# Kernel tuning notes

Hardware: AMD Instinct MI355X
Metric: run time of the kernel (lower is better)

## Reference

```python
import jax, jax.numpy as jnp
import numpy as np

NUM_EXPERTS = 32
TOP_K = 8
HIDDEN = 1536
INTER = 512


def setup_inputs() -> dict:
    key = jax.random.key(0)
    k1, k2, k3, k4 = jax.random.split(key, 4)
    hidden_states = jax.random.normal(k1, (4, 2048, HIDDEN), dtype=jnp.float32)
    # gate (router) weight: [E, H] as in nn.Linear(hidden, num_experts)
    gate_w = jax.random.normal(k2, (NUM_EXPERTS, HIDDEN), dtype=jnp.float32) * 0.02
    # fused gate+up projection per expert: [E, 2*I, H] (first I rows = gate/silu path)
    w13 = jax.random.normal(k3, (NUM_EXPERTS, 2 * INTER, HIDDEN), dtype=jnp.float32) * 0.02
    # down projection per expert: [E, H, I]
    w2 = jax.random.normal(k4, (NUM_EXPERTS, HIDDEN, INTER), dtype=jnp.float32) * 0.02
    return {"hidden_states": hidden_states, "gate_w": gate_w, "w13": w13, "w2": w2}


def _moe_forward(x, gate_w, w13, w2):
    orig_shape = x.shape
    x = x.reshape(-1, HIDDEN)            # [T, H]
    T = x.shape[0]

    # Router: softmax over all experts, then top-k, then renormalize.
    router_logits = x @ gate_w.T          # [T, E]
    probs = jax.nn.softmax(router_logits, axis=-1)
    topk_w, topk_idx = jax.lax.top_k(probs, TOP_K)        # [T, K]
    topk_w = topk_w / jnp.sum(topk_w, axis=-1, keepdims=True)

    # Scatter top-k weights into a dense [T, E] combine matrix (zeros elsewhere).
    expert_w = jnp.zeros((T, NUM_EXPERTS), dtype=x.dtype)
    expert_w = expert_w.at[jnp.arange(T)[:, None], topk_idx].add(topk_w)
    expert_w_eT = expert_w.T              # [E, T]

    def body(acc, ew):
        we, w13_e, w2_e = ew              # [T], [2I, H], [H, I]
        gu = x @ w13_e.T                  # [T, 2I]
        g, u = gu[:, :INTER], gu[:, INTER:]
        y = (jax.nn.silu(g) * u) @ w2_e.T  # [T, H]
        return acc + we[:, None] * y, None

    out, _ = jax.lax.scan(body, jnp.zeros_like(x), (expert_w_eT, w13, w2))
    return out.reshape(orig_shape)


def reference(hidden_states, gate_w, w13, w2):
    return _moe_forward(hidden_states, gate_w, w13, w2)
```

## Files before the change

kernel.cpp:

```cpp
#include <hip/hip_runtime.h>
#include <hip/hip_bf16.h>
#include <math.h>

#define NUM_EXPERTS 32
#define TOP_K 8
#define HIDDEN 1536
#define INTER 512

typedef __bf16 bf16_t;
typedef __bf16 bf16x8 __attribute__((ext_vector_type(8)));
typedef __bf16 bf16x4 __attribute__((ext_vector_type(4)));
typedef float f32x4 __attribute__((ext_vector_type(4)));

#define M_COUNTS    0
#define M_OFFSETS   32
#define M_CURSORS   96
#define M_NUMTILES  128
#define M_TILE_E    256
#define M_TILE_M0   1024
#define M_TILE_ROWS 2048
#define META_BYTES  16384

__device__ __forceinline__ void gld16(void* lds, const void* gsrc) {
  __builtin_amdgcn_global_load_lds(
      (const __attribute__((address_space(1))) void*)gsrc,
      (__attribute__((address_space(3))) void*)lds, 16, 0, 0);
}

__global__ __launch_bounds__(256) void k_cvt(
    const float* __restrict__ src, bf16_t* __restrict__ dst)
{
  size_t i = ((size_t)blockIdx.x * 256 + threadIdx.x) * 4;
  f32x4 v = *(const f32x4*)(src + i);
  bf16x4 o;
  o[0] = (bf16_t)v[0]; o[1] = (bf16_t)v[1]; o[2] = (bf16_t)v[2]; o[3] = (bf16_t)v[3];
  *(bf16x4*)(dst + i) = o;
}

__global__ __launch_bounds__(256) void k_tgw(
    const float* __restrict__ gw, float* __restrict__ gwT4)
{
  int tid = blockIdx.x * 256 + threadIdx.x;
  int e = tid / HIDDEN, k = tid % HIDDEN;
  gwT4[(k >> 2) * 128 + (e << 2) + (k & 3)] = gw[tid];
}

__global__ __launch_bounds__(64) void k_router(
    const float* __restrict__ x, const float* __restrict__ gwT4,
    int* __restrict__ meta, int* __restrict__ topk_idx, float* __restrict__ topk_w,
    bf16_t* __restrict__ x16)
{
  int t = blockIdx.x;
  int lane = threadIdx.x;
  int e = lane & 31, part = lane >> 5;
  const float* xrow = x + (size_t)t * HIDDEN;
  const f32x4* xr = (const f32x4*)(xrow + part * 768);
  const f32x4* gr = (const f32x4*)(gwT4 + part * 192 * 128 + e * 4);
  float s = 0.f;
#pragma unroll 4
  for (int i = 0; i < 192; ++i) {
    f32x4 xv = xr[i];
    f32x4 gv = gr[i * 32];
    s += xv[0] * gv[0] + xv[1] * gv[1] + xv[2] * gv[2] + xv[3] * gv[3];
  }
  s += __shfl_xor(s, 32);

  {
    const f32x4* xv4 = (const f32x4*)(xrow + lane * 24);
    bf16_t* xo = x16 + (size_t)t * HIDDEN + lane * 24;
#pragma unroll
    for (int i = 0; i < 6; ++i) {
      f32x4 v = xv4[i];
      bf16x4 o;
      o[0] = (bf16_t)v[0]; o[1] = (bf16_t)v[1]; o[2] = (bf16_t)v[2]; o[3] = (bf16_t)v[3];
      *(bf16x4*)(xo + i * 4) = o;
    }
  }

  float logit = s, rem = s;
  float m0 = 0.f, wsum = 0.f, my_l = 0.f;
  int my_e = 0;
#pragma unroll
  for (int k = 0; k < TOP_K; ++k) {
    float mx = rem;
#pragma unroll
    for (int off = 32; off >= 1; off >>= 1) mx = fmaxf(mx, __shfl_xor(mx, off));
    unsigned long long bal = __ballot(rem == mx);
    int src = __ffsll(bal) - 1;
    int ex = src & 31;
    float lv = __shfl(logit, ex);
    if (k == 0) m0 = mx;
    wsum += __expf(lv - m0);
    if (lane == k) { my_e = ex; my_l = lv; }
    if ((lane & 31) == ex) rem = -1e30f;
  }
  if (lane < TOP_K) {
    topk_idx[t * TOP_K + lane] = my_e;
    topk_w[t * TOP_K + lane] = __expf(my_l - m0) / wsum;
    atomicAdd(&meta[M_COUNTS + my_e], 1);
  }
}

__global__ void k_scan(int* __restrict__ meta)
{
  if (threadIdx.x != 0 || blockIdx.x != 0) return;
  int off = 0, nt = 0;
  for (int e = 0; e < NUM_EXPERTS; ++e) {
    int n = meta[M_COUNTS + e];
    meta[M_OFFSETS + e] = off;
    meta[M_CURSORS + e] = off;
    int tn = (n + 127) >> 7;
    for (int i = 0; i < tn; ++i) {
      meta[M_TILE_E + nt] = e;
      meta[M_TILE_M0 + nt] = off + i * 128;
      meta[M_TILE_ROWS + nt] = min(128, n - i * 128);
      ++nt;
    }
    off += n;
  }
  meta[M_OFFSETS + NUM_EXPERTS] = off;
  meta[M_NUMTILES] = nt;
}

__global__ __launch_bounds__(256) void k_scatter(
    const int* __restrict__ topk_idx,
    int* __restrict__ meta, int* __restrict__ pair_token, int* __restrict__ pair_pos)
{
  int i = blockIdx.x * 256 + threadIdx.x;
  int e = topk_idx[i];
  int pos = atomicAdd(&meta[M_CURSORS + e], 1);
  pair_token[pos] = i >> 3;
  pair_pos[i] = pos;
}

__global__ __launch_bounds__(256, 3) void k_gemm1(
    const bf16_t* __restrict__ x, const bf16_t* __restrict__ w13,
    const int* __restrict__ meta, const int* __restrict__ pair_token,
    bf16_t* __restrict__ act)
{
  int numtiles = meta[M_NUMTILES];
  int xcd = blockIdx.x & 7, s = blockIdx.x >> 3;
  int chunk = (numtiles * 4 + 7) >> 3;
  if (s >= chunk) return;
  int W = xcd * chunk + s;
  int tile = W >> 2, nb = W & 3;
  if (tile >= numtiles) return;
  int e    = meta[M_TILE_E + tile];
  int m0   = meta[M_TILE_M0 + tile];
  int rows = meta[M_TILE_ROWS + tile];
  int n0g  = nb * 128;

  __shared__ __align__(16) char smem[49152];
  char* As = smem;
  char* Bs = smem + 16384;

  int tid = threadIdx.x;
  int lane = tid & 63, w = tid >> 6;
  int cd = lane & 7;
  int lrow = w * 8 + (lane >> 3);

  const bf16_t* a_src[4];
  const bf16_t* b_src[8];
#pragma unroll
  for (int i = 0; i < 4; ++i) {
    int r = i * 32 + lrow;
    int rr = (r < rows) ? r : 0;
    int tok = pair_token[m0 + rr];
    int cg = cd ^ (r & 7);
    a_src[i] = x + (size_t)tok * HIDDEN + cg * 8;
  }
#pragma unroll
  for (int i = 0; i < 8; ++i) {
    int r = i * 32 + lrow;
    int cg = cd ^ (r & 7);
    int gr = (r < 128) ? (n0g + r) : (512 + n0g + (r - 128));
    b_src[i] = w13 + (size_t)e * (2 * INTER) * HIDDEN + (size_t)gr * HIDDEN + cg * 8;
  }
  unsigned lds_off = w * 1024 + lane * 16;

  f32x4 acc[2][16] = {};
  int q = lane >> 4, cl = lane & 15;
  int arow0 = (w * 32 + cl) * 128;
  int arow1 = (w * 32 + 16 + cl) * 128;

  for (int k0 = 0; k0 < HIDDEN; k0 += 64) {
#pragma unroll
    for (int i = 0; i < 4; ++i) gld16(As + i * 4096 + lds_off, a_src[i] + k0);
#pragma unroll
    for (int i = 0; i < 8; ++i) gld16(Bs + i * 4096 + lds_off, b_src[i] + k0);
    __syncthreads();
#pragma unroll
    for (int ks = 0; ks < 2; ++ks) {
      int csw = ((ks * 4 + q) ^ (lane & 7)) * 16;
      bf16x8 a0 = *(const bf16x8*)(As + arow0 + csw);
      bf16x8 a1 = *(const bf16x8*)(As + arow1 + csw);
#pragma unroll
      for (int in = 0; in < 16; ++in) {
        bf16x8 b = *(const bf16x8*)(Bs + (in * 16 + cl) * 128 + csw);
        acc[0][in] = __builtin_amdgcn_mfma_f32_16x16x32_bf16(a0, b, acc[0][in], 0, 0, 0);
        acc[1][in] = __builtin_amdgcn_mfma_f32_16x16x32_bf16(a1, b, acc[1][in], 0, 0, 0);
      }
    }
    __syncthreads();
  }

  char* tb = smem + w * 8704;
#pragma unroll
  for (int im = 0; im < 2; ++im) {
#pragma unroll
    for (int reg = 0; reg < 4; ++reg) {
      int r = im * 16 + q * 4 + reg;
#pragma unroll
      for (int in = 0; in < 8; ++in) {
        float g = acc[im][in][reg];
        float u = acc[im][in + 8][reg];
        float a = (g / (1.f + __expf(-g))) * u;
        *(bf16_t*)(tb + r * 272 + (in * 16 + cl) * 2) = (bf16_t)a;
      }
    }
  }
#pragma unroll
  for (int i = 0; i < 8; ++i) {
    int r = (lane >> 4) + i * 4;
    bf16x8 v = *(const bf16x8*)(tb + r * 272 + (lane & 15) * 16);
    int row = w * 32 + r;
    if (row < rows)
      *(bf16x8*)(act + (size_t)(m0 + row) * INTER + n0g + (lane & 15) * 8) = v;
  }
}

__global__ __launch_bounds__(256, 3) void k_gemm2(
    const bf16_t* __restrict__ act, const bf16_t* __restrict__ w2,
    const int* __restrict__ meta, bf16_t* __restrict__ y, int n0base)
{
  int numtiles = meta[M_NUMTILES];
  int xcd = blockIdx.x & 7, s = blockIdx.x >> 3;
  int chunk = (numtiles * 3 + 7) >> 3;
  if (s >= chunk) return;
  int W = xcd * chunk + s;
  int tile = W / 3, nb = W - tile * 3;
  if (tile >= numtiles) return;
  int e    = meta[M_TILE_E + tile];
  int m0   = meta[M_TILE_M0 + tile];
  int rows = meta[M_TILE_ROWS + tile];
  int n0l  = nb * 256;
  int n0   = n0base + n0l;

  __shared__ __align__(16) char smem[49152];
  char* As = smem;
  char* Bs = smem + 16384;

  int tid = threadIdx.x;
  int lane = tid & 63, w = tid >> 6;
  int cd = lane & 7;
  int lrow = w * 8 + (lane >> 3);

  const bf16_t* a_src[4];
  const bf16_t* b_src[8];
#pragma unroll
  for (int i = 0; i < 4; ++i) {
    int r = i * 32 + lrow;
    int rr = (r < rows) ? r : 0;
    int cg = cd ^ (r & 7);
    a_src[i] = act + (size_t)(m0 + rr) * INTER + cg * 8;
  }
#pragma unroll
  for (int i = 0; i < 8; ++i) {
    int r = i * 32 + lrow;
    int cg = cd ^ (r & 7);
    b_src[i] = w2 + (size_t)e * HIDDEN * INTER + (size_t)(n0 + r) * INTER + cg * 8;
  }
  unsigned lds_off = w * 1024 + lane * 16;

  f32x4 acc[2][16] = {};
  int q = lane >> 4, cl = lane & 15;
  int arow0 = (w * 32 + cl) * 128;
  int arow1 = (w * 32 + 16 + cl) * 128;

  for (int k0 = 0; k0 < INTER; k0 += 64) {
#pragma unroll
    for (int i = 0; i < 4; ++i) gld16(As + i * 4096 + lds_off, a_src[i] + k0);
#pragma unroll
    for (int i = 0; i < 8; ++i) gld16(Bs + i * 4096 + lds_off, b_src[i] + k0);
    __syncthreads();
#pragma unroll
    for (int ks = 0; ks < 2; ++ks) {
      int csw = ((ks * 4 + q) ^ (lane & 7)) * 16;
      bf16x8 a0 = *(const bf16x8*)(As + arow0 + csw);
      bf16x8 a1 = *(const bf16x8*)(As + arow1 + csw);
#pragma unroll
      for (int in = 0; in < 16; ++in) {
        bf16x8 b = *(const bf16x8*)(Bs + (in * 16 + cl) * 128 + csw);
        acc[0][in] = __builtin_amdgcn_mfma_f32_16x16x32_bf16(a0, b, acc[0][in], 0, 0, 0);
        acc[1][in] = __builtin_amdgcn_mfma_f32_16x16x32_bf16(a1, b, acc[1][in], 0, 0, 0);
      }
    }
    __syncthreads();
  }

  char* tb = smem + w * 8448;
#pragma unroll
  for (int im = 0; im < 2; ++im) {
#pragma unroll
    for (int reg = 0; reg < 4; ++reg) {
      int r = q * 4 + reg;
#pragma unroll
      for (int in = 0; in < 16; ++in)
        *(bf16_t*)(tb + r * 528 + (in * 16 + cl) * 2) = (bf16_t)acc[im][in][reg];
    }
#pragma unroll
    for (int i = 0; i < 8; ++i) {
      int r = (lane >> 5) + i * 2;
      bf16x8 v = *(const bf16x8*)(tb + r * 528 + (lane & 31) * 16);
      int row = w * 32 + im * 16 + r;
      if (row < rows)
        *(bf16x8*)(y + (size_t)(m0 + row) * 768 + n0l + (lane & 31) * 8) = v;
    }
  }
}

__global__ __launch_bounds__(256) void k_combine(
    const bf16_t* __restrict__ y, const int* __restrict__ pair_pos,
    const float* __restrict__ topk_w, float* __restrict__ out, int colbase)
{
  int idx = blockIdx.x * 256 + threadIdx.x;
  int t = idx / 96, c = idx % 96;
  const int*   pp = pair_pos + t * 8;
  const float* tw = topk_w + t * 8;
  f32x4 sa = {}, sb = {};
#pragma unroll
  for (int k = 0; k < 8; ++k) {
    int pos = pp[k];
    float wgt = tw[k];
    bf16x8 v = *(const bf16x8*)(y + (size_t)pos * 768 + c * 8);
    sa[0] += wgt * (float)v[0]; sa[1] += wgt * (float)v[1];
    sa[2] += wgt * (float)v[2]; sa[3] += wgt * (float)v[3];
    sb[0] += wgt * (float)v[4]; sb[1] += wgt * (float)v[5];
    sb[2] += wgt * (float)v[6]; sb[3] += wgt * (float)v[7];
  }
  float* o = out + (size_t)t * HIDDEN + colbase + c * 8;
  *(f32x4*)o = sa;
  *(f32x4*)(o + 4) = sb;
}

extern "C" void kernel_launch(void* const* d_in, const int* in_sizes, int n_in,
                              void* d_out, int out_size, void* d_ws, size_t ws_size,
                              hipStream_t stream)
{
  const float* x   = (const float*)d_in[0];
  const float* gw  = (const float*)d_in[1];
  const float* w13 = (const float*)d_in[2];
  const float* w2  = (const float*)d_in[3];
  float* out = (float*)d_out;

  const int T = in_sizes[0] / HIDDEN;
  const int P = T * TOP_K;
  const size_t NX   = (size_t)T * HIDDEN;
  const size_t NW13 = (size_t)NUM_EXPERTS * 2 * INTER * HIDDEN;
  const size_t NW2  = (size_t)NUM_EXPERTS * HIDDEN * INTER;

  char* ws = (char*)d_ws;
  int*    meta        = (int*)ws;
  int*    topk_idx    = (int*)(ws + META_BYTES);
  float*  topk_w      = (float*)(ws + META_BYTES + (size_t)P * 4);
  int*    pair_token  = (int*)(ws + META_BYTES + (size_t)P * 8);
  int*    pair_pos    = (int*)(ws + META_BYTES + (size_t)P * 12);
  float*  gwT4        = (float*)(ws + (1536u << 10));
  size_t off = 2u << 20;
  bf16_t* w2_16  = (bf16_t*)(ws + off); off += NW2 * 2;
  bf16_t* act    = (bf16_t*)(ws + off); off += (size_t)P * INTER * 2;
  size_t y_off = off;
  bf16_t* x16    = (bf16_t*)(ws + off); off += NX * 2;
  bf16_t* w13_16 = (bf16_t*)(ws + off);
  bf16_t* y      = (bf16_t*)(ws + y_off);

  hipMemsetAsync(meta, 0, 32 * sizeof(int), stream);

  k_tgw<<<(HIDDEN * NUM_EXPERTS) / 256, 256, 0, stream>>>(gw, gwT4);
  k_cvt<<<NW13 / 1024, 256, 0, stream>>>(w13, w13_16);
  k_cvt<<<NW2 / 1024, 256, 0, stream>>>(w2, w2_16);

  k_router<<<T, 64, 0, stream>>>(x, gwT4, meta, topk_idx, topk_w, x16);
  k_scan<<<1, 64, 0, stream>>>(meta);
  k_scatter<<<P / 256, 256, 0, stream>>>(topk_idx, meta, pair_token, pair_pos);

  k_gemm1<<<544 * 4, 256, 0, stream>>>(x16, w13_16, meta, pair_token, act);

  k_gemm2<<<544 * 3, 256, 0, stream>>>(act, w2_16, meta, y, 0);
  k_combine<<<(T * 96) / 256, 256, 0, stream>>>(y, pair_pos, topk_w, out, 0);
  k_gemm2<<<544 * 3, 256, 0, stream>>>(act, w2_16, meta, y, 768);
  k_combine<<<(T * 96) / 256, 256, 0, stream>>>(y, pair_pos, topk_w, out, 768);
}
```

Before: 1.187 ms.

## Replace global-atomic routing with block histograms, single-pass down GEMM, wider conversion

```diff
diff --git a/kernel.cpp b/kernel.cpp
--- a/kernel.cpp
+++ b/kernel.cpp
@@ -14,7 +14,6 @@
 
 #define M_COUNTS    0
 #define M_OFFSETS   32
-#define M_CURSORS   96
 #define M_NUMTILES  128
 #define M_TILE_E    256
 #define M_TILE_M0   1024
@@ -30,11 +29,13 @@
 __global__ __launch_bounds__(256) void k_cvt(
     const float* __restrict__ src, bf16_t* __restrict__ dst)
 {
-  size_t i = ((size_t)blockIdx.x * 256 + threadIdx.x) * 4;
-  f32x4 v = *(const f32x4*)(src + i);
-  bf16x4 o;
-  o[0] = (bf16_t)v[0]; o[1] = (bf16_t)v[1]; o[2] = (bf16_t)v[2]; o[3] = (bf16_t)v[3];
-  *(bf16x4*)(dst + i) = o;
+  size_t i = ((size_t)blockIdx.x * 256 + threadIdx.x) * 8;
+  f32x4 a = *(const f32x4*)(src + i);
+  f32x4 b = *(const f32x4*)(src + i + 4);
+  bf16x8 o;
+  o[0] = (bf16_t)a[0]; o[1] = (bf16_t)a[1]; o[2] = (bf16_t)a[2]; o[3] = (bf16_t)a[3];
+  o[4] = (bf16_t)b[0]; o[5] = (bf16_t)b[1]; o[6] = (bf16_t)b[2]; o[7] = (bf16_t)b[3];
+  *(bf16x8*)(dst + i) = o;
 }
 
 __global__ __launch_bounds__(256) void k_tgw(
@@ -47,7 +48,7 @@
 
 __global__ __launch_bounds__(64) void k_router(
     const float* __restrict__ x, const float* __restrict__ gwT4,
-    int* __restrict__ meta, int* __restrict__ topk_idx, float* __restrict__ topk_w,
+    int* __restrict__ topk_idx, float* __restrict__ topk_w,
     bf16_t* __restrict__ x16)
 {
   int t = blockIdx.x;
@@ -97,18 +98,36 @@
   if (lane < TOP_K) {
     topk_idx[t * TOP_K + lane] = my_e;
     topk_w[t * TOP_K + lane] = __expf(my_l - m0) / wsum;
-    atomicAdd(&meta[M_COUNTS + my_e], 1);
-  }
-}
-
-__global__ void k_scan(int* __restrict__ meta)
+  }
+}
+
+__global__ __launch_bounds__(1024) void k_hist(
+    const int* __restrict__ topk_idx, int* __restrict__ hist)
+{
+  __shared__ int h[NUM_EXPERTS];
+  int t = threadIdx.x;
+  if (t < NUM_EXPERTS) h[t] = 0;
+  __syncthreads();
+  int e = topk_idx[(size_t)blockIdx.x * 1024 + t];
+  atomicAdd(&h[e], 1);
+  __syncthreads();
+  if (t < NUM_EXPERTS) hist[blockIdx.x * NUM_EXPERTS + t] = h[t];
+}
+
+__global__ void k_scan(int* __restrict__ meta, const int* __restrict__ hist,
+                       int* __restrict__ base, int nhb)
 {
   if (threadIdx.x != 0 || blockIdx.x != 0) return;
   int off = 0, nt = 0;
   for (int e = 0; e < NUM_EXPERTS; ++e) {
-    int n = meta[M_COUNTS + e];
+    int run = off;
+    for (int b = 0; b < nhb; ++b) {
+      base[b * NUM_EXPERTS + e] = run;
+      run += hist[b * NUM_EXPERTS + e];
+    }
+    int n = run - off;
+    meta[M_COUNTS + e] = n;
     meta[M_OFFSETS + e] = off;
-    meta[M_CURSORS + e] = off;
     int tn = (n + 127) >> 7;
     for (int i = 0; i < tn; ++i) {
       meta[M_TILE_E + nt] = e;
@@ -122,13 +141,18 @@
   meta[M_NUMTILES] = nt;
 }
 
-__global__ __launch_bounds__(256) void k_scatter(
-    const int* __restrict__ topk_idx,
-    int* __restrict__ meta, int* __restrict__ pair_token, int* __restrict__ pair_pos)
-{
-  int i = blockIdx.x * 256 + threadIdx.x;
+__global__ __launch_bounds__(1024) void k_scatter(
+    const int* __restrict__ topk_idx, const int* __restrict__ base,
+    int* __restrict__ pair_token, int* __restrict__ pair_pos)
+{
+  __shared__ int h[NUM_EXPERTS];
+  int t = threadIdx.x;
+  if (t < NUM_EXPERTS) h[t] = 0;
+  __syncthreads();
+  int i = blockIdx.x * 1024 + t;
   int e = topk_idx[i];
-  int pos = atomicAdd(&meta[M_CURSORS + e], 1);
+  int r = atomicAdd(&h[e], 1);
+  int pos = base[blockIdx.x * NUM_EXPERTS + e] + r;
   pair_token[pos] = i >> 3;
   pair_pos[i] = pos;
 }
@@ -231,14 +255,15 @@
 
 __global__ __launch_bounds__(256, 3) void k_gemm2(
     const bf16_t* __restrict__ act, const bf16_t* __restrict__ w2,
-    const int* __restrict__ meta, bf16_t* __restrict__ y, int n0base)
+    const int* __restrict__ meta, bf16_t* __restrict__ y,
+    int n0base, int NBp, int ypitch)
 {
   int numtiles = meta[M_NUMTILES];
   int xcd = blockIdx.x & 7, s = blockIdx.x >> 3;
-  int chunk = (numtiles * 3 + 7) >> 3;
+  int chunk = (numtiles * NBp + 7) >> 3;
   if (s >= chunk) return;
   int W = xcd * chunk + s;
-  int tile = W / 3, nb = W - tile * 3;
+  int tile = W / NBp, nb = W - tile * NBp;
   if (tile >= numtiles) return;
   int e    = meta[M_TILE_E + tile];
   int m0   = meta[M_TILE_M0 + tile];
@@ -314,17 +339,19 @@
       bf16x8 v = *(const bf16x8*)(tb + r * 528 + (lane & 31) * 16);
       int row = w * 32 + im * 16 + r;
       if (row < rows)
-        *(bf16x8*)(y + (size_t)(m0 + row) * 768 + n0l + (lane & 31) * 8) = v;
+        *(bf16x8*)(y + (size_t)(m0 + row) * ypitch + n0l + (lane & 31) * 8) = v;
     }
   }
 }
 
 __global__ __launch_bounds__(256) void k_combine(
     const bf16_t* __restrict__ y, const int* __restrict__ pair_pos,
-    const float* __restrict__ topk_w, float* __restrict__ out, int colbase)
+    const float* __restrict__ topk_w, float* __restrict__ out,
+    int colbase, int CP)
 {
   int idx = blockIdx.x * 256 + threadIdx.x;
-  int t = idx / 96, c = idx % 96;
+  int cpg = CP >> 3;
+  int t = idx / cpg, c = idx % cpg;
   const int*   pp = pair_pos + t * 8;
   const float* tw = topk_w + t * 8;
   f32x4 sa = {}, sb = {};
@@ -332,7 +359,7 @@
   for (int k = 0; k < 8; ++k) {
     int pos = pp[k];
     float wgt = tw[k];
-    bf16x8 v = *(const bf16x8*)(y + (size_t)pos * 768 + c * 8);
+    bf16x8 v = *(const bf16x8*)(y + (size_t)pos * CP + c * 8);
     sa[0] += wgt * (float)v[0]; sa[1] += wgt * (float)v[1];
     sa[2] += wgt * (float)v[2]; sa[3] += wgt * (float)v[3];
     sb[0] += wgt * (float)v[4]; sb[1] += wgt * (float)v[5];
@@ -355,6 +382,8 @@
 
   const int T = in_sizes[0] / HIDDEN;
   const int P = T * TOP_K;
+  const int HB = P / 1024;
+  const int NTMAX = (P >> 7) + NUM_EXPERTS;
   const size_t NX   = (size_t)T * HIDDEN;
   const size_t NW13 = (size_t)NUM_EXPERTS * 2 * INTER * HIDDEN;
   const size_t NW2  = (size_t)NUM_EXPERTS * HIDDEN * INTER;
@@ -365,6 +394,8 @@
   float*  topk_w      = (float*)(ws + META_BYTES + (size_t)P * 4);
   int*    pair_token  = (int*)(ws + META_BYTES + (size_t)P * 8);
   int*    pair_pos    = (int*)(ws + META_BYTES + (size_t)P * 12);
+  int*    hist        = (int*)(ws + META_BYTES + (size_t)P * 16);
+  int*    base        = hist + HB * NUM_EXPERTS;
   float*  gwT4        = (float*)(ws + (1536u << 10));
   size_t off = 2u << 20;
   bf16_t* w2_16  = (bf16_t*)(ws + off); off += NW2 * 2;
@@ -374,20 +405,26 @@
   bf16_t* w13_16 = (bf16_t*)(ws + off);
   bf16_t* y      = (bf16_t*)(ws + y_off);
 
-  hipMemsetAsync(meta, 0, 32 * sizeof(int), stream);
+  bool onepass = ws_size >= y_off + (size_t)P * HIDDEN * 2 + (4u << 20);
 
   k_tgw<<<(HIDDEN * NUM_EXPERTS) / 256, 256, 0, stream>>>(gw, gwT4);
-  k_cvt<<<NW13 / 1024, 256, 0, stream>>>(w13, w13_16);
-  k_cvt<<<NW2 / 1024, 256, 0, stream>>>(w2, w2_16);
-
-  k_router<<<T, 64, 0, stream>>>(x, gwT4, meta, topk_idx, topk_w, x16);
-  k_scan<<<1, 64, 0, stream>>>(meta);
-  k_scatter<<<P / 256, 256, 0, stream>>>(topk_idx, meta, pair_token, pair_pos);
-
-  k_gemm1<<<544 * 4, 256, 0, stream>>>(x16, w13_16, meta, pair_token, act);
-
-  k_gemm2<<<544 * 3, 256, 0, stream>>>(act, w2_16, meta, y, 0);
-  k_combine<<<(T * 96) / 256, 256, 0, stream>>>(y, pair_pos, topk_w, out, 0);
-  k_gemm2<<<544 * 3, 256, 0, stream>>>(act, w2_16, meta, y, 768);
-  k_combine<<<(T * 96) / 256, 256, 0, stream>>>(y, pair_pos, topk_w, out, 768);
-}
+  k_cvt<<<NW13 / 2048, 256, 0, stream>>>(w13, w13_16);
+  k_cvt<<<NW2 / 2048, 256, 0, stream>>>(w2, w2_16);
+
+  k_router<<<T, 64, 0, stream>>>(x, gwT4, topk_idx, topk_w, x16);
+  k_hist<<<HB, 1024, 0, stream>>>(topk_idx, hist);
+  k_scan<<<1, 64, 0, stream>>>(meta, hist, base, HB);
+  k_scatter<<<HB, 1024, 0, stream>>>(topk_idx, base, pair_token, pair_pos);
+
+  k_gemm1<<<NTMAX * 4, 256, 0, stream>>>(x16, w13_16, meta, pair_token, act);
+
+  if (onepass) {
+    k_gemm2<<<NTMAX * 6, 256, 0, stream>>>(act, w2_16, meta, y, 0, 6, 1536);
+    k_combine<<<(T * 192) / 256, 256, 0, stream>>>(y, pair_pos, topk_w, out, 0, 1536);
+  } else {
+    k_gemm2<<<NTMAX * 3, 256, 0, stream>>>(act, w2_16, meta, y, 0, 3, 768);
+    k_combine<<<(T * 96) / 256, 256, 0, stream>>>(y, pair_pos, topk_w, out, 0, 768);
+    k_gemm2<<<NTMAX * 3, 256, 0, stream>>>(act, w2_16, meta, y, 768, 3, 768);
+    k_combine<<<(T * 96) / 256, 256, 0, stream>>>(y, pair_pos, topk_w, out, 768, 768);
+  }
+}
```

After: 1.097 ms. 1.08x faster.
